# Performance work log

Hardware: AMD Instinct MI355X
Metric: run time of the kernel (lower is better)

Reference implementation:

```python
import jax, jax.numpy as jnp
import numpy as np

N_HEADS = 16
D_EMBED = 1024
HEAD_DIM = D_EMBED // N_HEADS


def setup_inputs() -> dict:
    key = jax.random.key(0)
    ks = jax.random.split(key, 9)
    s = 1.0 / np.sqrt(D_EMBED)
    def lin(kw, kb):
        W = jax.random.uniform(kw, (D_EMBED, D_EMBED), jnp.float32, -s, s)
        b = jax.random.uniform(kb, (D_EMBED,), jnp.float32, -s, s)
        return W, b
    q_w, q_b = lin(ks[0], ks[1])
    k_w, k_b = lin(ks[2], ks[3])
    v_w, v_b = lin(ks[4], ks[5])
    o_w, o_b = lin(ks[6], ks[7])
    x = jax.random.normal(ks[8], (4, 2048, D_EMBED), jnp.float32)
    return {"x": x, "q_w": q_w, "q_b": q_b, "k_w": k_w, "k_b": k_b,
            "v_w": v_w, "v_b": v_b, "o_w": o_w, "o_b": o_b}


def reference(x, q_w, q_b, k_w, k_b, v_w, v_b, o_w, o_b):
    B, S, _ = x.shape
    # projections; W stored as [in, out] so y = x @ W + b (matches nn.Linear math)
    def split_heads(y):
        return y.reshape(B, S, N_HEADS, HEAD_DIM).transpose(0, 2, 1, 3)  # [B,H,S,D]
    q = split_heads(x @ q_w + q_b)
    k = split_heads(x @ k_w + k_b)
    v = split_heads(x @ v_w + v_b)
    scale = 1.0 / np.sqrt(HEAD_DIM).astype(np.float32)
    scores = jnp.einsum('bhqd,bhkd->bhqk', q, k) * scale  # [B,H,S,S]
    weights = jax.nn.softmax(scores, axis=-1)
    attn = jnp.einsum('bhqk,bhkd->bhqd', weights, v)  # [B,H,S,D]
    attn = attn.transpose(0, 2, 1, 3).reshape(B, S, D_EMBED)
    return attn @ o_w + o_b
```

## Files before the change

### kernel.cpp

```cpp
#include <hip/hip_runtime.h>
#include <hip/hip_bf16.h>
#include <math.h>

typedef __attribute__((ext_vector_type(8))) short bf16x8;
typedef __attribute__((ext_vector_type(4))) float f32x4;

#define D_EMBED 1024
#define SEQ 2048
#define NH 16
#define HD 64
#define QSCALE 0.1803368801111204f

__device__ __forceinline__ short f2bf(float f) {
    union { float f; unsigned u; } v; v.f = f;
    return (short)((v.u + 0x7FFFu + ((v.u >> 16) & 1u)) >> 16);
}

__device__ __forceinline__ unsigned pk_bf16(float a, float b) {
#if __has_builtin(__builtin_amdgcn_cvt_pk_bf16_f32)
    typedef __attribute__((ext_vector_type(2))) __bf16 vbf2;
    union { vbf2 v; unsigned u; } c;
    c.v = __builtin_amdgcn_cvt_pk_bf16_f32(a, b);
    return c.u;
#else
    return (unsigned)(unsigned short)f2bf(a) | ((unsigned)(unsigned short)f2bf(b) << 16);
#endif
}

__device__ __forceinline__ float exp2f_(float x) {
#if __has_builtin(__builtin_amdgcn_exp2f)
    return __builtin_amdgcn_exp2f(x);
#else
    return __expf(x * 0.6931471805599453f);
#endif
}

typedef __attribute__((address_space(1))) const void gvoid_t;
typedef __attribute__((address_space(3))) void lvoid_t;
__device__ __forceinline__ void glds16(const void* g, void* l) {
    __builtin_amdgcn_global_load_lds((gvoid_t*)g, (lvoid_t*)l, 16, 0, 0);
}

__global__ __launch_bounds__(256) void xconv_kernel(const float* __restrict__ x,
                                                    short* __restrict__ xb)
{
    size_t i = ((size_t)blockIdx.x * 256 + threadIdx.x) * 8;
    float4 f0 = *(const float4*)(x + i);
    float4 f1 = *(const float4*)(x + i + 4);
    uint4 o;
    o.x = pk_bf16(f0.x, f0.y); o.y = pk_bf16(f0.z, f0.w);
    o.z = pk_bf16(f1.x, f1.y); o.w = pk_bf16(f1.z, f1.w);
    *(uint4*)(xb + i) = o;
}

__global__ __launch_bounds__(256) void wtrans_kernel(
    const float* __restrict__ w0, const float* __restrict__ w1,
    const float* __restrict__ w2, const float* __restrict__ w3,
    short* __restrict__ wt)
{
    __shared__ float tile[64][65];
    const float* W = (blockIdx.z == 0) ? w0 : (blockIdx.z == 1) ? w1
                   : (blockIdx.z == 2) ? w2 : w3;
    short* out = wt + (size_t)blockIdx.z * D_EMBED * D_EMBED;
    int k0 = blockIdx.x * 64, n0 = blockIdx.y * 64;
    #pragma unroll
    for (int i = 0; i < 16; i++) {
        int idx = threadIdx.x + i * 256; int r = idx >> 6, c = idx & 63;
        tile[r][c] = W[(size_t)(k0 + r) * D_EMBED + n0 + c];
    }
    __syncthreads();
    #pragma unroll
    for (int i = 0; i < 16; i++) {
        int idx = threadIdx.x + i * 256; int r = idx >> 6, c = idx & 63;
        out[(size_t)(n0 + r) * D_EMBED + k0 + c] = f2bf(tile[c][r]);
    }
}

__global__ __launch_bounds__(256) void gemm_qkv_kernel(
    const short* __restrict__ xb, const short* __restrict__ wt,
    const float* __restrict__ qb, const float* __restrict__ kb, const float* __restrict__ vb,
    short* __restrict__ qo, short* __restrict__ ko, short* __restrict__ vto)
{
    __shared__ __attribute__((aligned(16))) short As[128][32];
    __shared__ __attribute__((aligned(16))) short Bs[128][32];
    __shared__ __attribute__((aligned(16))) short Es[64][136];
    const int tid = threadIdx.x;
    const int lane = tid & 63, wv = tid >> 6;
    const int l16 = lane & 15, quad = lane >> 4;
    const int wm = (wv & 1) * 64, wn = (wv >> 1) * 64;
    const int m0 = blockIdx.y * 128, n0 = blockIdx.x * 128;

    const short* aptr0 = xb + (size_t)(m0 + (tid >> 2)) * D_EMBED + (tid & 3) * 8;
    const short* aptr1 = aptr0 + (size_t)64 * D_EMBED;
    const short* bptr0 = wt + (size_t)(n0 + (tid >> 2)) * D_EMBED + (tid & 3) * 8;
    const short* bptr1 = bptr0 + (size_t)64 * D_EMBED;
    char* aldsb = (char*)&As[0][0] + wv * 1024;
    char* bldsb = (char*)&Bs[0][0] + wv * 1024;

    f32x4 acc[4][4];
    #pragma unroll
    for (int a = 0; a < 4; a++)
        #pragma unroll
        for (int b = 0; b < 4; b++) acc[a][b] = (f32x4){0.f, 0.f, 0.f, 0.f};

    for (int k0 = 0; k0 < D_EMBED; k0 += 32) {
        __syncthreads();
        glds16(aptr0 + k0, aldsb);
        glds16(aptr1 + k0, aldsb + 4096);
        glds16(bptr0 + k0, bldsb);
        glds16(bptr1 + k0, bldsb + 4096);
        __syncthreads();
        bf16x8 af[4], bfr[4];
        #pragma unroll
        for (int mi = 0; mi < 4; mi++) af[mi]  = *(const bf16x8*)&As[wm + mi * 16 + l16][quad * 8];
        #pragma unroll
        for (int ni = 0; ni < 4; ni++) bfr[ni] = *(const bf16x8*)&Bs[wn + ni * 16 + l16][quad * 8];
        #pragma unroll
        for (int mi = 0; mi < 4; mi++)
            #pragma unroll
            for (int ni = 0; ni < 4; ni++)
                acc[mi][ni] = __builtin_amdgcn_mfma_f32_16x16x32_bf16(af[mi], bfr[ni], acc[mi][ni], 0, 0, 0);
    }

    const int zz = n0 >> 10;
    if (zz == 2) {
        const int b = m0 >> 11, st0 = m0 & 2047;
        const int hbase = (n0 & 1023) >> 6;
        #pragma unroll
        for (int h2 = 0; h2 < 2; h2++) {
            __syncthreads();
            if ((wv >> 1) == h2) {
                #pragma unroll
                for (int mi = 0; mi < 4; mi++) {
                    int sbase = (wv & 1) * 64 + mi * 16 + quad * 4;
                    #pragma unroll
                    for (int ni = 0; ni < 4; ni++) {
                        int d = ni * 16 + l16;
                        float bv = vb[(n0 & 1023) + h2 * 64 + d];
                        uint2 pw;
                        pw.x = pk_bf16(acc[mi][ni][0] + bv, acc[mi][ni][1] + bv);
                        pw.y = pk_bf16(acc[mi][ni][2] + bv, acc[mi][ni][3] + bv);
                        *(uint2*)&Es[d][sbase] = pw;
                    }
                }
            }
            __syncthreads();
            const int h = hbase + h2;
            #pragma unroll
            for (int j = 0; j < 4; j++) {
                int d = j * 16 + (tid >> 4);
                int sc = (tid & 15) * 8;
                bf16x8 vv = *(const bf16x8*)&Es[d][sc];
                *(bf16x8*)(vto + ((size_t)(b * NH + h) * HD + d) * SEQ + st0 + sc) = vv;
            }
        }
    } else {
        const int ncol0 = (n0 & 1023) + wn;
        const float* bias = (zz == 0) ? qb : kb;
        #pragma unroll
        for (int mi = 0; mi < 4; mi++)
            #pragma unroll
            for (int ni = 0; ni < 4; ni++)
                #pragma unroll
                for (int rg = 0; rg < 4; rg++) {
                    int row = m0 + wm + mi * 16 + quad * 4 + rg;
                    int col = ncol0 + ni * 16 + l16;
                    float v = acc[mi][ni][rg] + bias[col];
                    int b = row >> 11, s = row & 2047, h = col >> 6, d = col & 63;
                    if (zz == 0) qo[(((size_t)(b * NH + h)) * SEQ + s) * HD + d] = f2bf(v * QSCALE);
                    else         ko[(((size_t)(b * NH + h)) * SEQ + s) * HD + d] = f2bf(v);
                }
    }
}

__global__ __launch_bounds__(256) void flash_kernel(
    const short* __restrict__ Q, const short* __restrict__ K,
    const short* __restrict__ Vt, short* __restrict__ attn,
    short* __restrict__ Op0, short* __restrict__ Op1,
    float* __restrict__ lp0, float* __restrict__ lp1,
    int ktn, int mode)
{
    __shared__ __attribute__((aligned(16))) short Ks[64][64];
    __shared__ __attribute__((aligned(16))) short Vs[64][64];
    __shared__ __attribute__((aligned(16))) short Ps[4][64][72];
    const int bh = blockIdx.y, qt = blockIdx.x;
    const int kt0 = blockIdx.z * ktn;
    const int tid = threadIdx.x, lane = tid & 63, wv = tid >> 6;
    const int l16 = lane & 15, quad = lane >> 4;
    const int sw = l16 & 7;

    bf16x8 qf[4][2];
    #pragma unroll
    for (int g = 0; g < 4; g++) {
        const short* qp = Q + ((size_t)bh * SEQ + qt * 256 + wv * 64 + g * 16 + l16) * HD;
        qf[g][0] = *(const bf16x8*)(qp + quad * 8);
        qf[g][1] = *(const bf16x8*)(qp + 32 + quad * 8);
    }

    const int sr = tid >> 3;
    const int scg = (tid & 7) ^ (sr & 7);
    const short* kp0 = K  + ((size_t)bh * SEQ + sr) * HD + scg * 8;
    const short* vp0 = Vt + ((size_t)bh * HD + sr) * SEQ + scg * 8;
    char* kldsb = (char*)&Ks[0][0] + wv * 1024;
    char* vldsb = (char*)&Vs[0][0] + wv * 1024;

    float lsum[4] = {0.f, 0.f, 0.f, 0.f};
    f32x4 oacc[4][4];
    #pragma unroll
    for (int g = 0; g < 4; g++)
        #pragma unroll
        for (int di = 0; di < 4; di++) oacc[g][di] = (f32x4){0.f, 0.f, 0.f, 0.f};

    for (int kt = kt0; kt < kt0 + ktn; kt += 64) {
        __syncthreads();
        glds16(kp0 + (size_t)kt * HD, kldsb);
        glds16(kp0 + (size_t)(kt + 32) * HD, kldsb + 4096);
        glds16(vp0 + kt, vldsb);
        glds16(vp0 + (size_t)32 * SEQ + kt, vldsb + 4096);
        __syncthreads();

        bf16x8 kf[4][2];
        #pragma unroll
        for (int ni = 0; ni < 4; ni++) {
            kf[ni][0] = *(const bf16x8*)&Ks[ni * 16 + l16][((quad    ) ^ sw) * 8];
            kf[ni][1] = *(const bf16x8*)&Ks[ni * 16 + l16][((quad + 4) ^ sw) * 8];
        }

        #pragma unroll
        for (int g = 0; g < 4; g++) {
            f32x4 sacc[4];
            #pragma unroll
            for (int ni = 0; ni < 4; ni++) {
                sacc[ni] = (f32x4){0.f, 0.f, 0.f, 0.f};
                sacc[ni] = __builtin_amdgcn_mfma_f32_16x16x32_bf16(kf[ni][0], qf[g][0], sacc[ni], 0, 0, 0);
                sacc[ni] = __builtin_amdgcn_mfma_f32_16x16x32_bf16(kf[ni][1], qf[g][1], sacc[ni], 0, 0, 0);
            }
            short* prow = &Ps[wv][g * 16 + l16][0];
            float ps = 0.f;
            #pragma unroll
            for (int ni = 0; ni < 4; ni++) {
                float p0 = exp2f_(sacc[ni][0]);
                float p1 = exp2f_(sacc[ni][1]);
                float p2 = exp2f_(sacc[ni][2]);
                float p3 = exp2f_(sacc[ni][3]);
                ps += (p0 + p1) + (p2 + p3);
                uint2 pw; pw.x = pk_bf16(p0, p1); pw.y = pk_bf16(p2, p3);
                *(uint2*)(prow + ni * 16 + quad * 4) = pw;
            }
            lsum[g] += ps;
        }

        bf16x8 vf[4][2];
        #pragma unroll
        for (int di = 0; di < 4; di++) {
            vf[di][0] = *(const bf16x8*)&Vs[di * 16 + l16][((quad    ) ^ sw) * 8];
            vf[di][1] = *(const bf16x8*)&Vs[di * 16 + l16][((quad + 4) ^ sw) * 8];
        }
        #pragma unroll
        for (int g = 0; g < 4; g++) {
            const short* prow = &Ps[wv][g * 16 + l16][0];
            bf16x8 pf0 = *(const bf16x8*)(prow + quad * 8);
            bf16x8 pf1 = *(const bf16x8*)(prow + 32 + quad * 8);
            #pragma unroll
            for (int di = 0; di < 4; di++) {
                oacc[g][di] = __builtin_amdgcn_mfma_f32_16x16x32_bf16(pf0, vf[di][0], oacc[g][di], 0, 0, 0);
                oacc[g][di] = __builtin_amdgcn_mfma_f32_16x16x32_bf16(pf1, vf[di][1], oacc[g][di], 0, 0, 0);
            }
        }
    }

    const int b = bh >> 4, h = bh & 15;
    short* Oz = blockIdx.z ? Op1 : Op0;
    float* lz = blockIdx.z ? lp1 : lp0;
    #pragma unroll
    for (int g = 0; g < 4; g++) {
        float l = lsum[g];
        l += __shfl_xor(l, 16);
        l += __shfl_xor(l, 32);
        if (mode) {
            if (quad == 0) lz[(size_t)bh * SEQ + qt * 256 + wv * 64 + g * 16 + l16] = l;
            #pragma unroll
            for (int di = 0; di < 4; di++)
                #pragma unroll
                for (int rg = 0; rg < 4; rg++) {
                    int s = qt * 256 + wv * 64 + g * 16 + quad * 4 + rg;
                    int col = h * HD + di * 16 + l16;
                    Oz[((size_t)b * SEQ + s) * D_EMBED + col] = f2bf(oacc[g][di][rg]);
                }
        } else {
            float rl[4];
            #pragma unroll
            for (int rg = 0; rg < 4; rg++) rl[rg] = 1.0f / __shfl(l, quad * 4 + rg);
            #pragma unroll
            for (int di = 0; di < 4; di++)
                #pragma unroll
                for (int rg = 0; rg < 4; rg++) {
                    int s = qt * 256 + wv * 64 + g * 16 + quad * 4 + rg;
                    int col = h * HD + di * 16 + l16;
                    attn[((size_t)b * SEQ + s) * D_EMBED + col] = f2bf(oacc[g][di][rg] * rl[rg]);
                }
        }
    }
}

__global__ __launch_bounds__(256) void combine_kernel(
    const short* __restrict__ Op0, const short* __restrict__ Op1,
    const float* __restrict__ lp0, const float* __restrict__ lp1,
    short* __restrict__ attn)
{
    size_t i = (size_t)blockIdx.x * 256 + threadIdx.x;
    int r = (int)(i >> 7);
    int c8 = ((int)i & 127) * 8;
    int h = c8 >> 6, b = r >> 11, s = r & 2047;
    float l = lp0[(size_t)(b * NH + h) * SEQ + s] + lp1[(size_t)(b * NH + h) * SEQ + s];
    float rl = 1.0f / l;
    uint4 a0 = *(const uint4*)(Op0 + i * 8);
    uint4 a1 = *(const uint4*)(Op1 + i * 8);
    uint4 o;
    unsigned ua[4] = {a0.x, a0.y, a0.z, a0.w};
    unsigned ub[4] = {a1.x, a1.y, a1.z, a1.w};
    unsigned uo[4];
    #pragma unroll
    for (int j = 0; j < 4; j++) {
        union { unsigned u; float f; } f0l, f0h, f1l, f1h;
        f0l.u = (ua[j] & 0xffffu) << 16; f0h.u = ua[j] & 0xffff0000u;
        f1l.u = (ub[j] & 0xffffu) << 16; f1h.u = ub[j] & 0xffff0000u;
        uo[j] = pk_bf16((f0l.f + f1l.f) * rl, (f0h.f + f1h.f) * rl);
    }
    o.x = uo[0]; o.y = uo[1]; o.z = uo[2]; o.w = uo[3];
    *(uint4*)(attn + i * 8) = o;
}

__global__ __launch_bounds__(256) void gemm_out_kernel(
    const short* __restrict__ attn, const short* __restrict__ wt_o,
    const float* __restrict__ ob, float* __restrict__ out)
{
    __shared__ __attribute__((aligned(16))) short As[128][32];
    __shared__ __attribute__((aligned(16))) short Bs[128][32];
    const int tid = threadIdx.x;
    const int lane = tid & 63, wv = tid >> 6;
    const int l16 = lane & 15, quad = lane >> 4;
    const int wm = (wv & 1) * 64, wn = (wv >> 1) * 64;
    const int m0 = blockIdx.y * 128, n0 = blockIdx.x * 128;

    const short* aptr0 = attn + (size_t)(m0 + (tid >> 2)) * D_EMBED + (tid & 3) * 8;
    const short* aptr1 = aptr0 + (size_t)64 * D_EMBED;
    const short* bptr0 = wt_o + (size_t)(n0 + (tid >> 2)) * D_EMBED + (tid & 3) * 8;
    const short* bptr1 = bptr0 + (size_t)64 * D_EMBED;
    char* aldsb = (char*)&As[0][0] + wv * 1024;
    char* bldsb = (char*)&Bs[0][0] + wv * 1024;

    f32x4 acc[4][4];
    #pragma unroll
    for (int a = 0; a < 4; a++)
        #pragma unroll
        for (int b = 0; b < 4; b++) acc[a][b] = (f32x4){0.f, 0.f, 0.f, 0.f};

    for (int k0 = 0; k0 < D_EMBED; k0 += 32) {
        __syncthreads();
        glds16(aptr0 + k0, aldsb);
        glds16(aptr1 + k0, aldsb + 4096);
        glds16(bptr0 + k0, bldsb);
        glds16(bptr1 + k0, bldsb + 4096);
        __syncthreads();
        bf16x8 af[4], bfr[4];
        #pragma unroll
        for (int mi = 0; mi < 4; mi++) af[mi]  = *(const bf16x8*)&As[wm + mi * 16 + l16][quad * 8];
        #pragma unroll
        for (int ni = 0; ni < 4; ni++) bfr[ni] = *(const bf16x8*)&Bs[wn + ni * 16 + l16][quad * 8];
        #pragma unroll
        for (int mi = 0; mi < 4; mi++)
            #pragma unroll
            for (int ni = 0; ni < 4; ni++)
                acc[mi][ni] = __builtin_amdgcn_mfma_f32_16x16x32_bf16(af[mi], bfr[ni], acc[mi][ni], 0, 0, 0);
    }

    #pragma unroll
    for (int mi = 0; mi < 4; mi++)
        #pragma unroll
        for (int ni = 0; ni < 4; ni++)
            #pragma unroll
            for (int rg = 0; rg < 4; rg++) {
                int row = m0 + wm + mi * 16 + quad * 4 + rg;
                int col = n0 + wn + ni * 16 + l16;
                out[(size_t)row * D_EMBED + col] = acc[mi][ni][rg] + ob[col];
            }
}

extern "C" void kernel_launch(void* const* d_in, const int* in_sizes, int n_in,
                              void* d_out, int out_size, void* d_ws, size_t ws_size,
                              hipStream_t stream) {
    const float* x  = (const float*)d_in[0];
    const float* qw = (const float*)d_in[1];
    const float* qb = (const float*)d_in[2];
    const float* kw = (const float*)d_in[3];
    const float* kb = (const float*)d_in[4];
    const float* vw = (const float*)d_in[5];
    const float* vb = (const float*)d_in[6];
    const float* ow = (const float*)d_in[7];
    const float* ob = (const float*)d_in[8];

    char* ws = (char*)d_ws;
    short* xb  = (short*)(ws);
    short* wt  = (short*)(ws + (size_t)(16 << 20));
    short* q   = (short*)(ws + (size_t)(24 << 20));
    short* k   = (short*)(ws + (size_t)(40 << 20));
    short* vt  = (short*)(ws + (size_t)(56 << 20));
    short* at  = xb;

    const bool split = ws_size >= (size_t)105 * 1024 * 1024;
    short* Op0 = (short*)(ws + (size_t)(72 << 20));
    short* Op1 = (short*)(ws + (size_t)(88 << 20));
    float* lp0 = (float*)(ws + (size_t)(104 << 20));
    float* lp1 = (float*)(ws + (size_t)(104 << 20) + SEQ * 64 * sizeof(float));

    xconv_kernel<<<4096, 256, 0, stream>>>(x, xb);
    wtrans_kernel<<<dim3(16, 16, 4), 256, 0, stream>>>(qw, kw, vw, ow, wt);
    gemm_qkv_kernel<<<dim3(24, 64), 256, 0, stream>>>(xb, wt, qb, kb, vb, q, k, vt);
    if (split) {
        flash_kernel<<<dim3(8, 64, 2), 256, 0, stream>>>(q, k, vt, at, Op0, Op1, lp0, lp1,
                                                         SEQ / 2, 1);
        combine_kernel<<<(8192 * 1024 / 8) / 256, 256, 0, stream>>>(Op0, Op1, lp0, lp1, at);
    } else {
        flash_kernel<<<dim3(8, 64, 1), 256, 0, stream>>>(q, k, vt, at, at, at, lp0, lp0,
                                                         SEQ, 0);
    }
    gemm_out_kernel<<<dim3(8, 64), 256, 0, stream>>>(at, wt + (size_t)3 * D_EMBED * D_EMBED, ob, (float*)d_out);
}
```

Baseline: 315.8 us.

## Split flash attention KV range three ways and halve out-GEMM tile width

The flash kernel gains a third split along the KV sequence (chunks of 704 keys, with the last chunk shorter), and a new three-way combine kernel merges the partial outputs. The three-way path is used only when the workspace holds at least 106MB. The output GEMM tile shrinks from 128x128 to 128x64, doubling the grid to 1024 blocks for better CU occupancy. The QKV GEMM shared buffers are unioned with the epilogue buffer to cut LDS use. In exchange there is more partial-output traffic to write and re-read, and one more combine input.

```diff
diff --git a/kernel.cpp b/kernel.cpp
--- a/kernel.cpp
+++ b/kernel.cpp
@@ -27,6 +27,13 @@
 #endif
 }
 
+__device__ __forceinline__ float bf2f_lo(unsigned u) {
+    union { unsigned u; float f; } v; v.u = (u & 0xffffu) << 16; return v.f;
+}
+__device__ __forceinline__ float bf2f_hi(unsigned u) {
+    union { unsigned u; float f; } v; v.u = u & 0xffff0000u; return v.f;
+}
+
 __device__ __forceinline__ float exp2f_(float x) {
 #if __has_builtin(__builtin_amdgcn_exp2f)
     return __builtin_amdgcn_exp2f(x);
@@ -81,9 +88,10 @@
     const float* __restrict__ qb, const float* __restrict__ kb, const float* __restrict__ vb,
     short* __restrict__ qo, short* __restrict__ ko, short* __restrict__ vto)
 {
-    __shared__ __attribute__((aligned(16))) short As[128][32];
-    __shared__ __attribute__((aligned(16))) short Bs[128][32];
-    __shared__ __attribute__((aligned(16))) short Es[64][136];
+    __shared__ __attribute__((aligned(16))) union ShQKV {
+        struct { short As[128][32]; short Bs[128][32]; } ab;
+        short Es[64][136];
+    } sh;
     const int tid = threadIdx.x;
     const int lane = tid & 63, wv = tid >> 6;
     const int l16 = lane & 15, quad = lane >> 4;
@@ -94,8 +102,8 @@
     const short* aptr1 = aptr0 + (size_t)64 * D_EMBED;
     const short* bptr0 = wt + (size_t)(n0 + (tid >> 2)) * D_EMBED + (tid & 3) * 8;
     const short* bptr1 = bptr0 + (size_t)64 * D_EMBED;
-    char* aldsb = (char*)&As[0][0] + wv * 1024;
-    char* bldsb = (char*)&Bs[0][0] + wv * 1024;
+    char* aldsb = (char*)&sh.ab.As[0][0] + wv * 1024;
+    char* bldsb = (char*)&sh.ab.Bs[0][0] + wv * 1024;
 
     f32x4 acc[4][4];
     #pragma unroll
@@ -112,9 +120,9 @@
         __syncthreads();
         bf16x8 af[4], bfr[4];
         #pragma unroll
-        for (int mi = 0; mi < 4; mi++) af[mi]  = *(const bf16x8*)&As[wm + mi * 16 + l16][quad * 8];
-        #pragma unroll
-        for (int ni = 0; ni < 4; ni++) bfr[ni] = *(const bf16x8*)&Bs[wn + ni * 16 + l16][quad * 8];
+        for (int mi = 0; mi < 4; mi++) af[mi]  = *(const bf16x8*)&sh.ab.As[wm + mi * 16 + l16][quad * 8];
+        #pragma unroll
+        for (int ni = 0; ni < 4; ni++) bfr[ni] = *(const bf16x8*)&sh.ab.Bs[wn + ni * 16 + l16][quad * 8];
         #pragma unroll
         for (int mi = 0; mi < 4; mi++)
             #pragma unroll
@@ -140,7 +148,7 @@
                         uint2 pw;
                         pw.x = pk_bf16(acc[mi][ni][0] + bv, acc[mi][ni][1] + bv);
                         pw.y = pk_bf16(acc[mi][ni][2] + bv, acc[mi][ni][3] + bv);
-                        *(uint2*)&Es[d][sbase] = pw;
+                        *(uint2*)&sh.Es[d][sbase] = pw;
                     }
                 }
             }
@@ -150,7 +158,7 @@
             for (int j = 0; j < 4; j++) {
                 int d = j * 16 + (tid >> 4);
                 int sc = (tid & 15) * 8;
-                bf16x8 vv = *(const bf16x8*)&Es[d][sc];
+                bf16x8 vv = *(const bf16x8*)&sh.Es[d][sc];
                 *(bf16x8*)(vto + ((size_t)(b * NH + h) * HD + d) * SEQ + st0 + sc) = vv;
             }
         }
@@ -176,15 +184,16 @@
 __global__ __launch_bounds__(256) void flash_kernel(
     const short* __restrict__ Q, const short* __restrict__ K,
     const short* __restrict__ Vt, short* __restrict__ attn,
-    short* __restrict__ Op0, short* __restrict__ Op1,
-    float* __restrict__ lp0, float* __restrict__ lp1,
-    int ktn, int mode)
+    short* __restrict__ Op0, short* __restrict__ Op1, short* __restrict__ Op2,
+    float* __restrict__ lp0, float* __restrict__ lp1, float* __restrict__ lp2,
+    int ktn_base, int mode)
 {
     __shared__ __attribute__((aligned(16))) short Ks[64][64];
     __shared__ __attribute__((aligned(16))) short Vs[64][64];
     __shared__ __attribute__((aligned(16))) short Ps[4][64][72];
     const int bh = blockIdx.y, qt = blockIdx.x;
-    const int kt0 = blockIdx.z * ktn;
+    const int kt0 = blockIdx.z * ktn_base;
+    const int kn = min(ktn_base, SEQ - kt0);
     const int tid = threadIdx.x, lane = tid & 63, wv = tid >> 6;
     const int l16 = lane & 15, quad = lane >> 4;
     const int sw = l16 & 7;
@@ -211,7 +220,7 @@
         #pragma unroll
         for (int di = 0; di < 4; di++) oacc[g][di] = (f32x4){0.f, 0.f, 0.f, 0.f};
 
-    for (int kt = kt0; kt < kt0 + ktn; kt += 64) {
+    for (int kt = kt0; kt < kt0 + kn; kt += 64) {
         __syncthreads();
         glds16(kp0 + (size_t)kt * HD, kldsb);
         glds16(kp0 + (size_t)(kt + 32) * HD, kldsb + 4096);
@@ -270,8 +279,8 @@
     }
 
     const int b = bh >> 4, h = bh & 15;
-    short* Oz = blockIdx.z ? Op1 : Op0;
-    float* lz = blockIdx.z ? lp1 : lp0;
+    short* Oz = (blockIdx.z == 0) ? Op0 : (blockIdx.z == 1) ? Op1 : Op2;
+    float* lz = (blockIdx.z == 0) ? lp0 : (blockIdx.z == 1) ? lp1 : lp2;
     #pragma unroll
     for (int g = 0; g < 4; g++) {
         float l = lsum[g];
@@ -303,7 +312,7 @@
     }
 }
 
-__global__ __launch_bounds__(256) void combine_kernel(
+__global__ __launch_bounds__(256) void combine2_kernel(
     const short* __restrict__ Op0, const short* __restrict__ Op1,
     const float* __restrict__ lp0, const float* __restrict__ lp1,
     short* __restrict__ attn)
@@ -312,21 +321,43 @@
     int r = (int)(i >> 7);
     int c8 = ((int)i & 127) * 8;
     int h = c8 >> 6, b = r >> 11, s = r & 2047;
-    float l = lp0[(size_t)(b * NH + h) * SEQ + s] + lp1[(size_t)(b * NH + h) * SEQ + s];
-    float rl = 1.0f / l;
+    size_t li = (size_t)(b * NH + h) * SEQ + s;
+    float rl = 1.0f / (lp0[li] + lp1[li]);
     uint4 a0 = *(const uint4*)(Op0 + i * 8);
     uint4 a1 = *(const uint4*)(Op1 + i * 8);
-    uint4 o;
     unsigned ua[4] = {a0.x, a0.y, a0.z, a0.w};
     unsigned ub[4] = {a1.x, a1.y, a1.z, a1.w};
-    unsigned uo[4];
-    #pragma unroll
-    for (int j = 0; j < 4; j++) {
-        union { unsigned u; float f; } f0l, f0h, f1l, f1h;
-        f0l.u = (ua[j] & 0xffffu) << 16; f0h.u = ua[j] & 0xffff0000u;
-        f1l.u = (ub[j] & 0xffffu) << 16; f1h.u = ub[j] & 0xffff0000u;
-        uo[j] = pk_bf16((f0l.f + f1l.f) * rl, (f0h.f + f1h.f) * rl);
-    }
+    uint4 o; unsigned uo[4];
+    #pragma unroll
+    for (int j = 0; j < 4; j++)
+        uo[j] = pk_bf16((bf2f_lo(ua[j]) + bf2f_lo(ub[j])) * rl,
+                        (bf2f_hi(ua[j]) + bf2f_hi(ub[j])) * rl);
+    o.x = uo[0]; o.y = uo[1]; o.z = uo[2]; o.w = uo[3];
+    *(uint4*)(attn + i * 8) = o;
+}
+
+__global__ __launch_bounds__(256) void combine3_kernel(
+    const short* __restrict__ Op0, const short* __restrict__ Op1, const short* __restrict__ Op2,
+    const float* __restrict__ lp0, const float* __restrict__ lp1, const float* __restrict__ lp2,
+    short* __restrict__ attn)
+{
+    size_t i = (size_t)blockIdx.x * 256 + threadIdx.x;
+    int r = (int)(i >> 7);
+    int c8 = ((int)i & 127) * 8;
+    int h = c8 >> 6, b = r >> 11, s = r & 2047;
+    size_t li = (size_t)(b * NH + h) * SEQ + s;
+    float rl = 1.0f / (lp0[li] + lp1[li] + lp2[li]);
+    uint4 a0 = *(const uint4*)(Op0 + i * 8);
+    uint4 a1 = *(const uint4*)(Op1 + i * 8);
+    uint4 a2 = *(const uint4*)(Op2 + i * 8);
+    unsigned ua[4] = {a0.x, a0.y, a0.z, a0.w};
+    unsigned ub[4] = {a1.x, a1.y, a1.z, a1.w};
+    unsigned uc[4] = {a2.x, a2.y, a2.z, a2.w};
+    uint4 o; unsigned uo[4];
+    #pragma unroll
+    for (int j = 0; j < 4; j++)
+        uo[j] = pk_bf16((bf2f_lo(ua[j]) + bf2f_lo(ub[j]) + bf2f_lo(uc[j])) * rl,
+                        (bf2f_hi(ua[j]) + bf2f_hi(ub[j]) + bf2f_hi(uc[j])) * rl);
     o.x = uo[0]; o.y = uo[1]; o.z = uo[2]; o.w = uo[3];
     *(uint4*)(attn + i * 8) = o;
 }
@@ -336,49 +367,47 @@
     const float* __restrict__ ob, float* __restrict__ out)
 {
     __shared__ __attribute__((aligned(16))) short As[128][32];
-    __shared__ __attribute__((aligned(16))) short Bs[128][32];
+    __shared__ __attribute__((aligned(16))) short Bs[64][32];
     const int tid = threadIdx.x;
     const int lane = tid & 63, wv = tid >> 6;
     const int l16 = lane & 15, quad = lane >> 4;
-    const int wm = (wv & 1) * 64, wn = (wv >> 1) * 64;
-    const int m0 = blockIdx.y * 128, n0 = blockIdx.x * 128;
+    const int wm = (wv & 1) * 64, wn = (wv >> 1) * 32;
+    const int m0 = blockIdx.y * 128, n0 = blockIdx.x * 64;
 
     const short* aptr0 = attn + (size_t)(m0 + (tid >> 2)) * D_EMBED + (tid & 3) * 8;
     const short* aptr1 = aptr0 + (size_t)64 * D_EMBED;
     const short* bptr0 = wt_o + (size_t)(n0 + (tid >> 2)) * D_EMBED + (tid & 3) * 8;
-    const short* bptr1 = bptr0 + (size_t)64 * D_EMBED;
     char* aldsb = (char*)&As[0][0] + wv * 1024;
     char* bldsb = (char*)&Bs[0][0] + wv * 1024;
 
-    f32x4 acc[4][4];
+    f32x4 acc[4][2];
     #pragma unroll
     for (int a = 0; a < 4; a++)
         #pragma unroll
-        for (int b = 0; b < 4; b++) acc[a][b] = (f32x4){0.f, 0.f, 0.f, 0.f};
+        for (int b = 0; b < 2; b++) acc[a][b] = (f32x4){0.f, 0.f, 0.f, 0.f};
 
     for (int k0 = 0; k0 < D_EMBED; k0 += 32) {
         __syncthreads();
         glds16(aptr0 + k0, aldsb);
         glds16(aptr1 + k0, aldsb + 4096);
         glds16(bptr0 + k0, bldsb);
-        glds16(bptr1 + k0, bldsb + 4096);
-        __syncthreads();
-        bf16x8 af[4], bfr[4];
+        __syncthreads();
+        bf16x8 af[4], bfr[2];
         #pragma unroll
         for (int mi = 0; mi < 4; mi++) af[mi]  = *(const bf16x8*)&As[wm + mi * 16 + l16][quad * 8];
         #pragma unroll
-        for (int ni = 0; ni < 4; ni++) bfr[ni] = *(const bf16x8*)&Bs[wn + ni * 16 + l16][quad * 8];
+        for (int ni = 0; ni < 2; ni++) bfr[ni] = *(const bf16x8*)&Bs[wn + ni * 16 + l16][quad * 8];
         #pragma unroll
         for (int mi = 0; mi < 4; mi++)
             #pragma unroll
-            for (int ni = 0; ni < 4; ni++)
+            for (int ni = 0; ni < 2; ni++)
                 acc[mi][ni] = __builtin_amdgcn_mfma_f32_16x16x32_bf16(af[mi], bfr[ni], acc[mi][ni], 0, 0, 0);
     }
 
     #pragma unroll
     for (int mi = 0; mi < 4; mi++)
         #pragma unroll
-        for (int ni = 0; ni < 4; ni++)
+        for (int ni = 0; ni < 2; ni++)
             #pragma unroll
             for (int rg = 0; rg < 4; rg++) {
                 int row = m0 + wm + mi * 16 + quad * 4 + rg;
@@ -406,24 +435,39 @@
     short* q   = (short*)(ws + (size_t)(24 << 20));
     short* k   = (short*)(ws + (size_t)(40 << 20));
     short* vt  = (short*)(ws + (size_t)(56 << 20));
-    short* at  = xb;
-
-    const bool split = ws_size >= (size_t)105 * 1024 * 1024;
+
+    const bool split3 = ws_size >= (size_t)106 * 1024 * 1024;
+    const bool split2 = !split3 && ws_size >= (size_t)105 * 1024 * 1024;
     short* Op0 = (short*)(ws + (size_t)(72 << 20));
     short* Op1 = (short*)(ws + (size_t)(88 << 20));
+    short* Op2 = xb;
     float* lp0 = (float*)(ws + (size_t)(104 << 20));
-    float* lp1 = (float*)(ws + (size_t)(104 << 20) + SEQ * 64 * sizeof(float));
+    float* lp1 = lp0 + (size_t)NH * 4 * SEQ;
+    float* lp2 = lp1 + (size_t)NH * 4 * SEQ;
 
     xconv_kernel<<<4096, 256, 0, stream>>>(x, xb);
     wtrans_kernel<<<dim3(16, 16, 4), 256, 0, stream>>>(qw, kw, vw, ow, wt);
     gemm_qkv_kernel<<<dim3(24, 64), 256, 0, stream>>>(xb, wt, qb, kb, vb, q, k, vt);
-    if (split) {
-        flash_kernel<<<dim3(8, 64, 2), 256, 0, stream>>>(q, k, vt, at, Op0, Op1, lp0, lp1,
-                                                         SEQ / 2, 1);
-        combine_kernel<<<(8192 * 1024 / 8) / 256, 256, 0, stream>>>(Op0, Op1, lp0, lp1, at);
+
+    short* at;
+    if (split3) {
+        at = q;
+        flash_kernel<<<dim3(8, 64, 3), 256, 0, stream>>>(q, k, vt, (short*)nullptr,
+                                                         Op0, Op1, Op2, lp0, lp1, lp2,
+                                                         704, 1);
+        combine3_kernel<<<(8192 * 1024 / 8) / 256, 256, 0, stream>>>(Op0, Op1, Op2,
+                                                                     lp0, lp1, lp2, at);
+    } else if (split2) {
+        at = xb;
+        flash_kernel<<<dim3(8, 64, 2), 256, 0, stream>>>(q, k, vt, (short*)nullptr,
+                                                         Op0, Op1, Op1, lp0, lp1, lp1,
+                                                         1024, 1);
+        combine2_kernel<<<(8192 * 1024 / 8) / 256, 256, 0, stream>>>(Op0, Op1, lp0, lp1, at);
     } else {
-        flash_kernel<<<dim3(8, 64, 1), 256, 0, stream>>>(q, k, vt, at, at, at, lp0, lp0,
+        at = xb;
+        flash_kernel<<<dim3(8, 64, 1), 256, 0, stream>>>(q, k, vt, at,
+                                                         at, at, at, lp0, lp0, lp0,
                                                          SEQ, 0);
     }
-    gemm_out_kernel<<<dim3(8, 64), 256, 0, stream>>>(at, wt + (size_t)3 * D_EMBED * D_EMBED, ob, (float*)d_out);
-}
+    gemm_out_kernel<<<dim3(16, 64), 256, 0, stream>>>(at, wt + (size_t)3 * D_EMBED * D_EMBED, ob, (float*)d_out);
+}
```

Result: slower. 326.1 us (+3.3%).
